# Kernel tuning notes

Measured on AMD Instinct MI355X. Metric: run time of the kernel, lower is better.

The kernel has to match this reference:

```python
import jax, jax.numpy as jnp
import numpy as np

NUM_EMBS = 1024
EMB_DIM = 128
Z_SHAPE = (16, 4096, EMB_DIM)


def setup_inputs() -> dict:
    key = jax.random.key(0)
    k_z, k_c = jax.random.split(key)
    z = jax.random.normal(k_z, Z_SHAPE, dtype=jnp.float32)
    # torch init: uniform(-1/num_embs, 1/num_embs)
    codebook = jax.random.uniform(
        k_c, (NUM_EMBS, EMB_DIM), dtype=jnp.float32,
        minval=-1.0 / NUM_EMBS, maxval=1.0 / NUM_EMBS)
    return {"z": z, "codebook": codebook}


def reference(z, codebook):
    """Vector quantization forward (nbooks=1, balance=False).

    Returns (z_q with straight-through estimator, quant_loss, commit_loss, indices).
    """
    K, D = codebook.shape
    zf = z.reshape(-1, D)  # [M, D]
    dist = (
        jnp.sum(zf * zf, axis=1, keepdims=True)
        - 2.0 * (zf @ codebook.T)
        + jnp.sum(codebook * codebook, axis=1)[None, :]
    )
    idx = jnp.argmin(dist, axis=1)  # [M]
    # one-hot @ codebook == gather (same math, efficient form)
    z_q = codebook[idx].reshape(z.shape)
    quant_loss = jnp.mean((jax.lax.stop_gradient(z_q) - z) ** 2, axis=-1)
    commit_loss = jnp.mean((z_q - jax.lax.stop_gradient(z)) ** 2, axis=-1)
    # straight-through estimator
    z_q_ste = z + jax.lax.stop_gradient(z_q - z)
    indices = idx.reshape(z.shape[:-1])
    return z_q_ste, quant_loss, commit_loss, indices
```

## Files before the change

kernel.cpp:

```cpp
#include <hip/hip_runtime.h>
#include <hip/hip_bf16.h>

namespace {
constexpr int D       = 128;
constexpr int K       = 1024;
constexpr int M_TOTAL = 65536;
constexpr int BM      = 128;
constexpr int NCT     = K / 16;
constexpr float TAU   = 5.0e-5f;
constexpr size_t WS_CN   = 0;
constexpr size_t WS_BH   = 4096;
constexpr size_t WS_BL   = 4096 + 262144;
constexpr size_t WS_REQ  = 4096 + 2 * 262144;
constexpr size_t WS_CBT  = WS_REQ;
constexpr size_t WS_REQ2 = WS_REQ + 524288;
}

typedef short bf16x8 __attribute__((ext_vector_type(8)));
typedef float f32x4  __attribute__((ext_vector_type(4)));

static __device__ __forceinline__ unsigned short bfbits(float x) {
  __hip_bfloat16 h = __float2bfloat16(x);
  return *reinterpret_cast<unsigned short*>(&h);
}
static __device__ __forceinline__ float bfhi2f(unsigned short h) {
  return __uint_as_float(((unsigned)h) << 16);
}
static __device__ __forceinline__ void split8(float4 a, float4 b,
                                              bf16x8& ph, bf16x8& pl) {
  float v[8] = {a.x, a.y, a.z, a.w, b.x, b.y, b.z, b.w};
#pragma unroll
  for (int e = 0; e < 8; ++e) {
    unsigned short h = bfbits(v[e]);
    unsigned short l = bfbits(v[e] - bfhi2f(h));
    ph[e] = (short)h;
    pl[e] = (short)l;
  }
}
static __device__ __forceinline__ float np_norm128(const float* p) {
  float r8[8];
#pragma unroll
  for (int j = 0; j < 8; ++j) r8[j] = __fmul_rn(p[j], p[j]);
  for (int i = 8; i < D; i += 8) {
#pragma unroll
    for (int j = 0; j < 8; ++j)
      r8[j] = __fadd_rn(r8[j], __fmul_rn(p[i + j], p[i + j]));
  }
  return __fadd_rn(__fadd_rn(__fadd_rn(r8[0], r8[1]), __fadd_rn(r8[2], r8[3])),
                   __fadd_rn(__fadd_rn(r8[4], r8[5]), __fadd_rn(r8[6], r8[7])));
}

__global__ void vq_prep_all(const float* __restrict__ cb, float* __restrict__ Cn,
                            int* __restrict__ cnt,
                            short* __restrict__ Bh, short* __restrict__ Bl,
                            float4* __restrict__ cbT4) {
  const int b = blockIdx.x, t = threadIdx.x;
  if (b < 4) {
    int k = b * 256 + t;
    if (b == 0 && t == 0) *cnt = 0;
    if (k < K) Cn[k] = np_norm128(cb + (size_t)k * D);
  } else if (b < 68) {
    int g = (b - 4) * 256 + t;
    int code = (g >> 8) * 16 + (g & 15);
    int d0   = ((g >> 6) & 3) * 32 + ((g >> 4) & 3) * 8;
    const float* p = cb + (size_t)code * D + d0;
    float4 a = *reinterpret_cast<const float4*>(p);
    float4 bb = *reinterpret_cast<const float4*>(p + 4);
    bf16x8 ph, pl;
    split8(a, bb, ph, pl);
    *reinterpret_cast<bf16x8*>(Bh + (size_t)g * 8) = ph;
    *reinterpret_cast<bf16x8*>(Bl + (size_t)g * 8) = pl;
  } else {
    int g = (b - 68) * 256 + t;
    int d = g >> 8, tt = g & 255;
    float4 v;
    v.x = cb[(size_t)(4 * tt + 0) * D + d];
    v.y = cb[(size_t)(4 * tt + 1) * D + d];
    v.z = cb[(size_t)(4 * tt + 2) * D + d];
    v.w = cb[(size_t)(4 * tt + 3) * D + d];
    cbT4[g] = v;
  }
}

__global__ __launch_bounds__(256, 2) void vq_score(
    const float* __restrict__ z, const float* __restrict__ Cn,
    const short* __restrict__ BhG, const short* __restrict__ BlG,
    float* __restrict__ out_iF, int* __restrict__ cnt, int* __restrict__ list) {
  __shared__ __align__(16) short Bbuf[8][8][512];
  __shared__ float CnS[K];

  const int t    = threadIdx.x;
  const int wave = t >> 6;
  const int lane = t & 63;
  const int col  = lane & 15;
  const int baseRow = blockIdx.x * BM;

  for (int i = t; i < K; i += 256) CnS[i] = Cn[i];

  bf16x8 ah[2][4], al[2][4];
#pragma unroll
  for (int set = 0; set < 2; ++set) {
    const float* zL = z + (size_t)(baseRow + wave * 32 + set * 16 + col) * D + (lane >> 4) * 8;
#pragma unroll
    for (int ks = 0; ks < 4; ++ks) {
      float4 a = *reinterpret_cast<const float4*>(zL + ks * 32);
      float4 b = *reinterpret_cast<const float4*>(zL + ks * 32 + 4);
      split8(a, b, ah[set][ks], al[set][ks]);
    }
  }

  float s1[2][4], s2[2][4]; int i1[2][4];
#pragma unroll
  for (int s = 0; s < 2; ++s)
#pragma unroll
    for (int i = 0; i < 4; ++i) {
      s1[s][i] = 3.402823466e+38f; s2[s][i] = 3.402823466e+38f; i1[s][i] = 0;
    }

#define STAGE(ct_, bi_)                                                             \
  { _Pragma("unroll")                                                               \
    for (int i_ = 0; i_ < 2; ++i_) {                                                \
      int c_  = wave * 2 + i_;                                                      \
      int p_  = c_ >> 2, ks_ = c_ & 3;                                              \
      const short* gsrc_ = (p_ ? BlG : BhG) +                                       \
                           (size_t)(((ct_) * 4 + ks_) * 64 + lane) * 8;             \
      __builtin_amdgcn_global_load_lds(                                             \
          (const __attribute__((address_space(1))) void*)gsrc_,                     \
          (__attribute__((address_space(3))) void*)&Bbuf[bi_][c_][0], 16, 0, 0);    \
    } }

#define COMP(bi_, ct_)                                                              \
  { bf16x8 bh_c[4], bl_c[4];                                                        \
    _Pragma("unroll")                                                               \
    for (int ks_ = 0; ks_ < 4; ++ks_) {                                             \
      bh_c[ks_] = *reinterpret_cast<const bf16x8*>(&Bbuf[bi_][ks_][lane * 8]);      \
      bl_c[ks_] = *reinterpret_cast<const bf16x8*>(&Bbuf[bi_][4 + ks_][lane * 8]);  \
    }                                                                               \
    const int code_ = (ct_) * 16 + col;                                             \
    const float cn_ = CnS[code_];                                                   \
    __builtin_amdgcn_s_setprio(1);                                                  \
    _Pragma("unroll")                                                               \
    for (int set_ = 0; set_ < 2; ++set_) {                                          \
      f32x4 aA = (f32x4){0.f,0.f,0.f,0.f};                                          \
      f32x4 aB = (f32x4){0.f,0.f,0.f,0.f};                                          \
      f32x4 aC = (f32x4){0.f,0.f,0.f,0.f};                                          \
      _Pragma("unroll")                                                             \
      for (int ks_ = 0; ks_ < 4; ++ks_) {                                           \
        aA = __builtin_amdgcn_mfma_f32_16x16x32_bf16(ah[set_][ks_], bh_c[ks_], aA, 0,0,0); \
        aB = __builtin_amdgcn_mfma_f32_16x16x32_bf16(ah[set_][ks_], bl_c[ks_], aB, 0,0,0); \
        aC = __builtin_amdgcn_mfma_f32_16x16x32_bf16(al[set_][ks_], bh_c[ks_], aC, 0,0,0); \
      }                                                                             \
      _Pragma("unroll")                                                             \
      for (int reg_ = 0; reg_ < 4; ++reg_) {                                        \
        float S = fmaf(-2.0f, (aA[reg_] + aB[reg_]) + aC[reg_], cn_);               \
        if (S < s1[set_][reg_]) { s2[set_][reg_] = s1[set_][reg_];                  \
                                  s1[set_][reg_] = S; i1[set_][reg_] = code_; }     \
        else if (S < s2[set_][reg_]) { s2[set_][reg_] = S; }                        \
      }                                                                             \
    }                                                                               \
    __builtin_amdgcn_s_setprio(0); }

#define PHASE(t_, bi_)                                                              \
  { asm volatile("s_waitcnt vmcnt(12)" ::: "memory");                               \
    __builtin_amdgcn_s_barrier();                                                   \
    __builtin_amdgcn_sched_barrier(0);                                              \
    COMP(bi_, t_);                                                                  \
    STAGE(((t_) + 7) & 63, ((bi_) + 7) & 7); }

  __syncthreads();
  STAGE(0, 0); STAGE(1, 1); STAGE(2, 2); STAGE(3, 3);
  STAGE(4, 4); STAGE(5, 5); STAGE(6, 6);
  for (int g = 0; g < NCT; g += 8) {
    PHASE(g + 0, 0);
    PHASE(g + 1, 1);
    PHASE(g + 2, 2);
    PHASE(g + 3, 3);
    PHASE(g + 4, 4);
    PHASE(g + 5, 5);
    PHASE(g + 6, 6);
    PHASE(g + 7, 7);
  }
#undef PHASE
#undef STAGE
#undef COMP

#pragma unroll
  for (int m = 1; m < 16; m <<= 1) {
#pragma unroll
    for (int set = 0; set < 2; ++set)
#pragma unroll
      for (int reg = 0; reg < 4; ++reg) {
        float os1 = __shfl_xor(s1[set][reg], m, 64);
        float os2 = __shfl_xor(s2[set][reg], m, 64);
        int   oi  = __shfl_xor(i1[set][reg], m, 64);
        if (os1 < s1[set][reg]) {
          s2[set][reg] = fminf(s1[set][reg], os2);
          s1[set][reg] = os1; i1[set][reg] = oi;
        } else {
          s2[set][reg] = fminf(s2[set][reg], os1);
        }
      }
  }

  if (col == 0) {
#pragma unroll
    for (int set = 0; set < 2; ++set)
#pragma unroll
      for (int reg = 0; reg < 4; ++reg) {
        int row = wave * 32 + set * 16 + (lane >> 4) * 4 + reg;
        size_t m = (size_t)baseRow + row;
        out_iF[m] = (float)i1[set][reg];
        if (s2[set][reg] - s1[set][reg] < TAU) {
          int p = atomicAdd(cnt, 1);
          if (p < M_TOTAL - 1) list[p] = (int)m;
        }
      }
  }
}

__global__ __launch_bounds__(256, 4) void vq_rescan_cbT(
    const float* __restrict__ z, const float4* __restrict__ cbT4,
    const float* __restrict__ Cn,
    const int* __restrict__ cnt, const int* __restrict__ list,
    float* __restrict__ out_iF) {
  __shared__ __align__(16) float Zs[D];
  __shared__ float sRed[256];
  __shared__ int   iRed[256];
  const int t = threadIdx.x;
  int n = *cnt; if (n > M_TOTAL - 1) n = M_TOTAL - 1;

  for (int it = blockIdx.x; it < n; it += gridDim.x) {
    const int row = list[it];
    if (t < 32) {
      reinterpret_cast<float4*>(Zs)[t] =
          reinterpret_cast<const float4*>(z + (size_t)row * D)[t];
    }
    __syncthreads();

    float a0 = 0.f, a1 = 0.f, a2 = 0.f, a3 = 0.f;
#pragma unroll 8
    for (int d = 0; d < D; ++d) {
      float  zv = Zs[d];
      float4 cv = cbT4[(d << 8) + t];
      a0 = fmaf(zv, cv.x, a0);
      a1 = fmaf(zv, cv.y, a1);
      a2 = fmaf(zv, cv.z, a2);
      a3 = fmaf(zv, cv.w, a3);
    }
    const float A = np_norm128(Zs);

    const int kb = t * 4;
    float bd = 3.402823466e+38f; int bi = 0;
    {
      float d0 = __fadd_rn(__fsub_rn(A, __fmul_rn(2.0f, a0)), Cn[kb + 0]);
      float d1 = __fadd_rn(__fsub_rn(A, __fmul_rn(2.0f, a1)), Cn[kb + 1]);
      float d2 = __fadd_rn(__fsub_rn(A, __fmul_rn(2.0f, a2)), Cn[kb + 2]);
      float d3 = __fadd_rn(__fsub_rn(A, __fmul_rn(2.0f, a3)), Cn[kb + 3]);
      if (d0 < bd) { bd = d0; bi = kb + 0; }
      if (d1 < bd) { bd = d1; bi = kb + 1; }
      if (d2 < bd) { bd = d2; bi = kb + 2; }
      if (d3 < bd) { bd = d3; bi = kb + 3; }
    }
    sRed[t] = bd; iRed[t] = bi;
    __syncthreads();
    for (int w = 128; w > 0; w >>= 1) {
      if (t < w) {
        float o = sRed[t + w]; int oi = iRed[t + w];
        if (o < sRed[t] || (o == sRed[t] && oi < iRed[t])) { sRed[t] = o; iRed[t] = oi; }
      }
      __syncthreads();
    }
    if (t == 0) out_iF[row] = (float)iRed[0];
    __syncthreads();
  }
}

__global__ __launch_bounds__(256) void vq_epi(
    const float* __restrict__ z, const float* __restrict__ cb,
    const float* __restrict__ out_iF,
    float* __restrict__ out_zq, float* __restrict__ out_q,
    float* __restrict__ out_c) {
  const int t = threadIdx.x;
  const int r = t >> 2, q = t & 3;
  const size_t m = (size_t)blockIdx.x * 64 + r;
  const int idx = (int)out_iF[m];
  const float4* cq = reinterpret_cast<const float4*>(cb + (size_t)idx * D);
  const float4* zr = reinterpret_cast<const float4*>(z + m * D);
  float4*       o4 = reinterpret_cast<float4*>(out_zq + m * D);
  float sum = 0.f;
#pragma unroll
  for (int e = 0; e < 8; ++e) {
    int d4 = q * 8 + e;
    float4 cv = cq[d4];
    float4 zv = zr[d4];
    float dx = cv.x - zv.x, dy = cv.y - zv.y, dz = cv.z - zv.z, dw = cv.w - zv.w;
    float4 st;
    st.x = zv.x + dx; st.y = zv.y + dy; st.z = zv.z + dz; st.w = zv.w + dw;
    o4[d4] = st;
    sum = fmaf(dx, dx, sum); sum = fmaf(dy, dy, sum);
    sum = fmaf(dz, dz, sum); sum = fmaf(dw, dw, sum);
  }
  sum += __shfl_xor(sum, 1, 64);
  sum += __shfl_xor(sum, 2, 64);
  if (q == 0) {
    float lv = sum * 0.0078125f;
    out_q[m] = lv;
    out_c[m] = lv;
  }
}

__global__ __launch_bounds__(256) void vq_main_fp32(
    const float* __restrict__ z, const float* __restrict__ cb,
    const float* __restrict__ Cn,
    float* __restrict__ out_zq, float* __restrict__ out_q,
    float* __restrict__ out_c, float* __restrict__ out_i) {
  __shared__ float Zt[64 * D];
  __shared__ float Ct[64 * D];
  __shared__ float Arow[64];
  __shared__ int   idxArr[64];

  const int t  = threadIdx.x;
  const int ty = t >> 4;
  const int tx = t & 15;
  const int baseRow = blockIdx.x * 64;

  for (int s = t; s < 64 * (D / 4); s += 256) {
    int r = s >> 5, d4 = s & 31;
    float4 v = reinterpret_cast<const float4*>(z)[(size_t)(baseRow + r) * (D / 4) + d4];
    int colx = d4 ^ (r & 7);
    *reinterpret_cast<float4*>(&Zt[r * D + colx * 4]) = v;
  }
  __syncthreads();

  if (t < 64) {
    const int rs = t & 7;
    float r8[8];
#pragma unroll
    for (int j = 0; j < 8; ++j) {
      float v = Zt[t * D + (((j >> 2) ^ rs) << 2) + (j & 3)];
      r8[j] = __fmul_rn(v, v);
    }
    for (int i = 8; i < D; i += 8) {
#pragma unroll
      for (int j = 0; j < 8; ++j) {
        int d = i + j;
        float v = Zt[t * D + (((d >> 2) ^ rs) << 2) + (d & 3)];
        r8[j] = __fadd_rn(r8[j], __fmul_rn(v, v));
      }
    }
    Arow[t] = __fadd_rn(__fadd_rn(__fadd_rn(r8[0], r8[1]), __fadd_rn(r8[2], r8[3])),
                        __fadd_rn(__fadd_rn(r8[4], r8[5]), __fadd_rn(r8[6], r8[7])));
  }

  float s1[4]; int i1[4];
#pragma unroll
  for (int i = 0; i < 4; ++i) { s1[i] = 3.402823466e+38f; i1[i] = 0; }

  const int zsw = ty & 7;
  const int csw = tx & 7;

  for (int kt = 0; kt < 16; ++kt) {
    __syncthreads();
    for (int s = t; s < 64 * (D / 4); s += 256) {
      int r = s >> 5, d4 = s & 31;
      float4 v = reinterpret_cast<const float4*>(cb)[(size_t)(kt * 64 + r) * (D / 4) + d4];
      int colx = d4 ^ (r & 7);
      *reinterpret_cast<float4*>(&Ct[r * D + colx * 4]) = v;
    }
    __syncthreads();

    float acc[4][4];
#pragma unroll
    for (int i = 0; i < 4; ++i)
#pragma unroll
      for (int j = 0; j < 4; ++j) acc[i][j] = 0.f;

    for (int d4 = 0; d4 < 32; ++d4) {
      float4 za[4], cv[4];
      int zc = (d4 ^ zsw) * 4;
      int cc = (d4 ^ csw) * 4;
#pragma unroll
      for (int i = 0; i < 4; ++i)
        za[i] = *reinterpret_cast<const float4*>(&Zt[(ty + 16 * i) * D + zc]);
#pragma unroll
      for (int j = 0; j < 4; ++j)
        cv[j] = *reinterpret_cast<const float4*>(&Ct[(tx + 16 * j) * D + cc]);
#pragma unroll
      for (int i = 0; i < 4; ++i)
#pragma unroll
        for (int j = 0; j < 4; ++j) {
          acc[i][j] = fmaf(za[i].x, cv[j].x, acc[i][j]);
          acc[i][j] = fmaf(za[i].y, cv[j].y, acc[i][j]);
          acc[i][j] = fmaf(za[i].z, cv[j].z, acc[i][j]);
          acc[i][j] = fmaf(za[i].w, cv[j].w, acc[i][j]);
        }
    }

    float ch[4]; int kg[4];
#pragma unroll
    for (int j = 0; j < 4; ++j) {
      kg[j] = kt * 64 + tx + 16 * j;
      ch[j] = Cn[kg[j]];
    }
#pragma unroll
    for (int i = 0; i < 4; ++i) {
      float a = Arow[ty + 16 * i];
#pragma unroll
      for (int j = 0; j < 4; ++j) {
        float dist = __fadd_rn(__fsub_rn(a, __fmul_rn(2.0f, acc[i][j])), ch[j]);
        if (dist < s1[i]) { s1[i] = dist; i1[i] = kg[j]; }
      }
    }
  }

#pragma unroll
  for (int m = 1; m < 16; m <<= 1) {
#pragma unroll
    for (int i = 0; i < 4; ++i) {
      float os = __shfl_xor(s1[i], m, 64);
      int   oi = __shfl_xor(i1[i], m, 64);
      if (os < s1[i] || (os == s1[i] && oi < i1[i])) { s1[i] = os; i1[i] = oi; }
    }
  }

  if (tx == 0) {
#pragma unroll
    for (int i = 0; i < 4; ++i) idxArr[ty + 16 * i] = i1[i];
  }
  __syncthreads();

  {
    int r = t >> 2, q = t & 3;
    int idx = idxArr[r];
    size_t m = (size_t)baseRow + r;
    const float4* cq = reinterpret_cast<const float4*>(cb + (size_t)idx * D);
    const float4* zr = reinterpret_cast<const float4*>(z + m * D);
    float4*       o4 = reinterpret_cast<float4*>(out_zq + m * D);
    float sum = 0.f;
#pragma unroll
    for (int e = 0; e < 8; ++e) {
      int d4 = q * 8 + e;
      float4 cv = cq[d4];
      float4 zv = zr[d4];
      float dx = cv.x - zv.x, dy = cv.y - zv.y, dz = cv.z - zv.z, dw = cv.w - zv.w;
      float4 st;
      st.x = zv.x + dx; st.y = zv.y + dy; st.z = zv.z + dz; st.w = zv.w + dw;
      o4[d4] = st;
      sum = fmaf(dx, dx, sum); sum = fmaf(dy, dy, sum);
      sum = fmaf(dz, dz, sum); sum = fmaf(dw, dw, sum);
    }
    sum += __shfl_xor(sum, 1, 64);
    sum += __shfl_xor(sum, 2, 64);
    if (q == 0) {
      float lv = sum * 0.0078125f;
      out_q[m] = lv;
      out_c[m] = lv;
      out_i[m] = (float)idx;
    }
  }
}

extern "C" void kernel_launch(void* const* d_in, const int* in_sizes, int n_in,
                              void* d_out, int out_size, void* d_ws, size_t ws_size,
                              hipStream_t stream) {
  const float* z  = (const float*)d_in[0];
  const float* cb = (const float*)d_in[1];

  float* out0 = (float*)d_out;
  float* out1 = out0 + (size_t)M_TOTAL * D;
  float* out2 = out1 + M_TOTAL;
  float* out3 = out2 + M_TOTAL;

  float* Cn = (float*)((char*)d_ws + WS_CN);
  int* cnt  = (int*)out2;
  int* list = (int*)out2 + 1;

  if (ws_size >= WS_REQ2) {
    short*  Bh   = (short*)((char*)d_ws + WS_BH);
    short*  Bl   = (short*)((char*)d_ws + WS_BL);
    float4* cbT4 = (float4*)((char*)d_ws + WS_CBT);
    vq_prep_all<<<196, 256, 0, stream>>>(cb, Cn, cnt, Bh, Bl, cbT4);
    vq_score<<<M_TOTAL / BM, 256, 0, stream>>>(z, Cn, Bh, Bl, out3, cnt, list);
    vq_rescan_cbT<<<1024, 256, 0, stream>>>(z, cbT4, Cn, cnt, list, out3);
    vq_epi<<<M_TOTAL / 64, 256, 0, stream>>>(z, cb, out3, out0, out1, out2);
  } else {
    vq_prep_all<<<4, 256, 0, stream>>>(cb, Cn, cnt, nullptr, nullptr, nullptr);
    vq_main_fp32<<<M_TOTAL / 64, 256, 0, stream>>>(z, cb, Cn, out0, out1, out2, out3);
  }
}
```

Baseline: 115.3 us.

## Give each wave private double-buffered codebook tiles and drop block barriers

Previously the four waves cooperatively staged each codebook tile into a shared 8-deep LDS ring and synchronized with a block barrier every tile. Now each wave loads the full tile itself into its own double-buffered LDS region and waits only on its own vmcnt, removing s_barrier from the inner loop. This trades four times the global/L2 load traffic and a shallower prefetch depth (2 instead of 7) for no inter-wave synchronization.

Measured after the change: 120.2 us. 1.04x slower.

```diff
diff --git a/kernel.cpp b/kernel.cpp
--- a/kernel.cpp
+++ b/kernel.cpp
@@ -86,7 +86,7 @@
     const float* __restrict__ z, const float* __restrict__ Cn,
     const short* __restrict__ BhG, const short* __restrict__ BlG,
     float* __restrict__ out_iF, int* __restrict__ cnt, int* __restrict__ list) {
-  __shared__ __align__(16) short Bbuf[8][8][512];
+  __shared__ __align__(16) short Bbuf[4][2][8][512];
   __shared__ float CnS[K];
 
   const int t    = threadIdx.x;
@@ -117,24 +117,23 @@
       s1[s][i] = 3.402823466e+38f; s2[s][i] = 3.402823466e+38f; i1[s][i] = 0;
     }
 
-#define STAGE(ct_, bi_)                                                             \
+#define STAGE(ct_, db_)                                                             \
   { _Pragma("unroll")                                                               \
-    for (int i_ = 0; i_ < 2; ++i_) {                                                \
-      int c_  = wave * 2 + i_;                                                      \
+    for (int c_ = 0; c_ < 8; ++c_) {                                                \
       int p_  = c_ >> 2, ks_ = c_ & 3;                                              \
       const short* gsrc_ = (p_ ? BlG : BhG) +                                       \
                            (size_t)(((ct_) * 4 + ks_) * 64 + lane) * 8;             \
       __builtin_amdgcn_global_load_lds(                                             \
           (const __attribute__((address_space(1))) void*)gsrc_,                     \
-          (__attribute__((address_space(3))) void*)&Bbuf[bi_][c_][0], 16, 0, 0);    \
+          (__attribute__((address_space(3))) void*)&Bbuf[wave][db_][c_][0], 16, 0, 0); \
     } }
 
-#define COMP(bi_, ct_)                                                              \
+#define COMP(db_, ct_)                                                              \
   { bf16x8 bh_c[4], bl_c[4];                                                        \
     _Pragma("unroll")                                                               \
     for (int ks_ = 0; ks_ < 4; ++ks_) {                                             \
-      bh_c[ks_] = *reinterpret_cast<const bf16x8*>(&Bbuf[bi_][ks_][lane * 8]);      \
-      bl_c[ks_] = *reinterpret_cast<const bf16x8*>(&Bbuf[bi_][4 + ks_][lane * 8]);  \
+      bh_c[ks_] = *reinterpret_cast<const bf16x8*>(&Bbuf[wave][db_][ks_][lane * 8]);     \
+      bl_c[ks_] = *reinterpret_cast<const bf16x8*>(&Bbuf[wave][db_][4 + ks_][lane * 8]); \
     }                                                                               \
     const int code_ = (ct_) * 16 + col;                                             \
     const float cn_ = CnS[code_];                                                   \
@@ -160,27 +159,21 @@
     }                                                                               \
     __builtin_amdgcn_s_setprio(0); }
 
-#define PHASE(t_, bi_)                                                              \
-  { asm volatile("s_waitcnt vmcnt(12)" ::: "memory");                               \
-    __builtin_amdgcn_s_barrier();                                                   \
-    __builtin_amdgcn_sched_barrier(0);                                              \
-    COMP(bi_, t_);                                                                  \
-    STAGE(((t_) + 7) & 63, ((bi_) + 7) & 7); }
+#define WAIT8  { asm volatile("s_waitcnt vmcnt(8)" ::: "memory"); \
+                 __builtin_amdgcn_sched_barrier(0); }
+#define WAIT0  { asm volatile("s_waitcnt vmcnt(0)" ::: "memory"); \
+                 __builtin_amdgcn_sched_barrier(0); }
 
   __syncthreads();
-  STAGE(0, 0); STAGE(1, 1); STAGE(2, 2); STAGE(3, 3);
-  STAGE(4, 4); STAGE(5, 5); STAGE(6, 6);
-  for (int g = 0; g < NCT; g += 8) {
-    PHASE(g + 0, 0);
-    PHASE(g + 1, 1);
-    PHASE(g + 2, 2);
-    PHASE(g + 3, 3);
-    PHASE(g + 4, 4);
-    PHASE(g + 5, 5);
-    PHASE(g + 6, 6);
-    PHASE(g + 7, 7);
-  }
-#undef PHASE
+  STAGE(0, 0); STAGE(1, 1);
+  for (int g = 0; g < NCT - 2; g += 2) {
+    WAIT8;  COMP(0, g);      STAGE(g + 2, 0);
+    WAIT8;  COMP(1, g + 1);  STAGE(g + 3, 1);
+  }
+  WAIT8;  COMP(0, NCT - 2);
+  WAIT0;  COMP(1, NCT - 1);
+#undef WAIT8
+#undef WAIT0
 #undef STAGE
 #undef COMP
 
```

## Fuse epilogue into score and rescan kernels, shrink staging ring to 4 buffers

Applied to the files above, without the earlier changes.

The separate epilogue kernel is removed. The score kernel now writes z_q, the loss and the index directly after its argmin reduction, and the rescan kernel rewrites those outputs for the ambiguous rows it recomputes. A tiny copy kernel duplicates quant_loss into commit_loss, because the out2 buffer is reused for the counter and list during scoring. The LDS staging ring is cut from 8 to 4 slots with matching waitcnt depth, which frees shared memory but reduces how far loads can run ahead, and the score kernel now carries extra epilogue global traffic.

Result: no change. 114.9 us (-0.3%).

```diff
diff --git a/kernel.cpp b/kernel.cpp
--- a/kernel.cpp
+++ b/kernel.cpp
@@ -83,11 +83,14 @@
 }
 
 __global__ __launch_bounds__(256, 2) void vq_score(
-    const float* __restrict__ z, const float* __restrict__ Cn,
+    const float* __restrict__ z, const float* __restrict__ cb,
+    const float* __restrict__ Cn,
     const short* __restrict__ BhG, const short* __restrict__ BlG,
+    float* __restrict__ out_zq, float* __restrict__ out_q,
     float* __restrict__ out_iF, int* __restrict__ cnt, int* __restrict__ list) {
-  __shared__ __align__(16) short Bbuf[8][8][512];
+  __shared__ __align__(16) short Bbuf[4][8][512];
   __shared__ float CnS[K];
+  __shared__ int   idxW[4][32];
 
   const int t    = threadIdx.x;
   const int wave = t >> 6;
@@ -161,24 +164,19 @@
     __builtin_amdgcn_s_setprio(0); }
 
 #define PHASE(t_, bi_)                                                              \
-  { asm volatile("s_waitcnt vmcnt(12)" ::: "memory");                               \
+  { asm volatile("s_waitcnt vmcnt(4)" ::: "memory");                                \
     __builtin_amdgcn_s_barrier();                                                   \
     __builtin_amdgcn_sched_barrier(0);                                              \
     COMP(bi_, t_);                                                                  \
-    STAGE(((t_) + 7) & 63, ((bi_) + 7) & 7); }
+    STAGE(((t_) + 3) & 63, ((bi_) + 3) & 3); }
 
   __syncthreads();
-  STAGE(0, 0); STAGE(1, 1); STAGE(2, 2); STAGE(3, 3);
-  STAGE(4, 4); STAGE(5, 5); STAGE(6, 6);
-  for (int g = 0; g < NCT; g += 8) {
+  STAGE(0, 0); STAGE(1, 1); STAGE(2, 2);
+  for (int g = 0; g < NCT; g += 4) {
     PHASE(g + 0, 0);
     PHASE(g + 1, 1);
     PHASE(g + 2, 2);
     PHASE(g + 3, 3);
-    PHASE(g + 4, 4);
-    PHASE(g + 5, 5);
-    PHASE(g + 6, 6);
-    PHASE(g + 7, 7);
   }
 #undef PHASE
 #undef STAGE
@@ -207,21 +205,48 @@
     for (int set = 0; set < 2; ++set)
 #pragma unroll
       for (int reg = 0; reg < 4; ++reg) {
-        int row = wave * 32 + set * 16 + (lane >> 4) * 4 + reg;
-        size_t m = (size_t)baseRow + row;
-        out_iF[m] = (float)i1[set][reg];
+        int wr = set * 16 + (lane >> 4) * 4 + reg;
+        idxW[wave][wr] = i1[set][reg];
         if (s2[set][reg] - s1[set][reg] < TAU) {
           int p = atomicAdd(cnt, 1);
-          if (p < M_TOTAL - 1) list[p] = (int)m;
+          if (p < M_TOTAL - 1) list[p] = (int)(baseRow + wave * 32 + wr);
         }
       }
   }
+
+  {
+    const int r = lane >> 1, q = lane & 1;
+    const size_t m = (size_t)baseRow + wave * 32 + r;
+    const int idx = idxW[wave][r];
+    const float4* cq = reinterpret_cast<const float4*>(cb + (size_t)idx * D) + q * 16;
+    const float4* zr = reinterpret_cast<const float4*>(z + m * D) + q * 16;
+    float4*       o4 = reinterpret_cast<float4*>(out_zq + m * D) + q * 16;
+    float sum = 0.f;
+#pragma unroll
+    for (int e = 0; e < 16; ++e) {
+      float4 cv = cq[e];
+      float4 zv = zr[e];
+      float dx = cv.x - zv.x, dy = cv.y - zv.y, dz = cv.z - zv.z, dw = cv.w - zv.w;
+      float4 st;
+      st.x = zv.x + dx; st.y = zv.y + dy; st.z = zv.z + dz; st.w = zv.w + dw;
+      o4[e] = st;
+      sum = fmaf(dx, dx, sum); sum = fmaf(dy, dy, sum);
+      sum = fmaf(dz, dz, sum); sum = fmaf(dw, dw, sum);
+    }
+    sum += __shfl_xor(sum, 1, 64);
+    if (q == 0) {
+      float lv = sum * 0.0078125f;
+      out_q[m]  = lv;
+      out_iF[m] = (float)idx;
+    }
+  }
 }
 
 __global__ __launch_bounds__(256, 4) void vq_rescan_cbT(
-    const float* __restrict__ z, const float4* __restrict__ cbT4,
-    const float* __restrict__ Cn,
+    const float* __restrict__ z, const float* __restrict__ cb,
+    const float4* __restrict__ cbT4, const float* __restrict__ Cn,
     const int* __restrict__ cnt, const int* __restrict__ list,
+    float* __restrict__ out_zq, float* __restrict__ out_q,
     float* __restrict__ out_iF) {
   __shared__ __align__(16) float Zs[D];
   __shared__ float sRed[256];
@@ -270,43 +295,30 @@
       }
       __syncthreads();
     }
-    if (t == 0) out_iF[row] = (float)iRed[0];
+    const int win = iRed[0];
+    if (t < 32) {
+      float4 zv = reinterpret_cast<const float4*>(Zs)[t];
+      float4 cv = reinterpret_cast<const float4*>(cb + (size_t)win * D)[t];
+      float dx = cv.x - zv.x, dy = cv.y - zv.y, dz = cv.z - zv.z, dw = cv.w - zv.w;
+      float4 st;
+      st.x = zv.x + dx; st.y = zv.y + dy; st.z = zv.z + dz; st.w = zv.w + dw;
+      reinterpret_cast<float4*>(out_zq + (size_t)row * D)[t] = st;
+      float sq = fmaf(dx, dx, fmaf(dy, dy, fmaf(dz, dz, dw * dw)));
+      sq += __shfl_xor(sq, 1, 64);  sq += __shfl_xor(sq, 2, 64);
+      sq += __shfl_xor(sq, 4, 64);  sq += __shfl_xor(sq, 8, 64);
+      sq += __shfl_xor(sq, 16, 64);
+      if (t == 0) {
+        out_q[row]  = sq * 0.0078125f;
+        out_iF[row] = (float)win;
+      }
+    }
     __syncthreads();
   }
 }
 
-__global__ __launch_bounds__(256) void vq_epi(
-    const float* __restrict__ z, const float* __restrict__ cb,
-    const float* __restrict__ out_iF,
-    float* __restrict__ out_zq, float* __restrict__ out_q,
-    float* __restrict__ out_c) {
-  const int t = threadIdx.x;
-  const int r = t >> 2, q = t & 3;
-  const size_t m = (size_t)blockIdx.x * 64 + r;
-  const int idx = (int)out_iF[m];
-  const float4* cq = reinterpret_cast<const float4*>(cb + (size_t)idx * D);
-  const float4* zr = reinterpret_cast<const float4*>(z + m * D);
-  float4*       o4 = reinterpret_cast<float4*>(out_zq + m * D);
-  float sum = 0.f;
-#pragma unroll
-  for (int e = 0; e < 8; ++e) {
-    int d4 = q * 8 + e;
-    float4 cv = cq[d4];
-    float4 zv = zr[d4];
-    float dx = cv.x - zv.x, dy = cv.y - zv.y, dz = cv.z - zv.z, dw = cv.w - zv.w;
-    float4 st;
-    st.x = zv.x + dx; st.y = zv.y + dy; st.z = zv.z + dz; st.w = zv.w + dw;
-    o4[d4] = st;
-    sum = fmaf(dx, dx, sum); sum = fmaf(dy, dy, sum);
-    sum = fmaf(dz, dz, sum); sum = fmaf(dw, dw, sum);
-  }
-  sum += __shfl_xor(sum, 1, 64);
-  sum += __shfl_xor(sum, 2, 64);
-  if (q == 0) {
-    float lv = sum * 0.0078125f;
-    out_q[m] = lv;
-    out_c[m] = lv;
-  }
+__global__ void vq_copy(const float* __restrict__ q, float* __restrict__ c) {
+  int m = blockIdx.x * 256 + threadIdx.x;
+  c[m] = q[m];
 }
 
 __global__ __launch_bounds__(256) void vq_main_fp32(
@@ -480,9 +492,11 @@
     short*  Bl   = (short*)((char*)d_ws + WS_BL);
     float4* cbT4 = (float4*)((char*)d_ws + WS_CBT);
     vq_prep_all<<<196, 256, 0, stream>>>(cb, Cn, cnt, Bh, Bl, cbT4);
-    vq_score<<<M_TOTAL / BM, 256, 0, stream>>>(z, Cn, Bh, Bl, out3, cnt, list);
-    vq_rescan_cbT<<<1024, 256, 0, stream>>>(z, cbT4, Cn, cnt, list, out3);
-    vq_epi<<<M_TOTAL / 64, 256, 0, stream>>>(z, cb, out3, out0, out1, out2);
+    vq_score<<<M_TOTAL / BM, 256, 0, stream>>>(z, cb, Cn, Bh, Bl,
+                                               out0, out1, out3, cnt, list);
+    vq_rescan_cbT<<<1024, 256, 0, stream>>>(z, cb, cbT4, Cn, cnt, list,
+                                            out0, out1, out3);
+    vq_copy<<<M_TOTAL / 256, 256, 0, stream>>>(out1, out2);
   } else {
     vq_prep_all<<<4, 256, 0, stream>>>(cb, Cn, cnt, nullptr, nullptr, nullptr);
     vq_main_fp32<<<M_TOTAL / 64, 256, 0, stream>>>(z, cb, Cn, out0, out1, out2, out3);
```
